# Optimization experiments

Measured on AMD Instinct MI355X. Metric: run time of the kernel, lower is better.

Reference implementation:

```python
import jax, jax.numpy as jnp
import numpy as np

N = 400_000   # active voxels
CIN = 64
COUT = 64
D = 192       # dense bounding volume side
K = 27        # 3x3x3 kernel taps


def _build_kmap():
    """Build per-tap neighbor index map [27, N], -1 where neighbor voxel is inactive.
    Mirrors fvdb's SparseConvPackInfo for stride=1, kernel=3, out_grid == in_grid."""
    rng = np.random.default_rng(0)
    coords = rng.integers(0, D, size=(int(N * 1.6), 3), dtype=np.int64)
    lin = coords[:, 0] * D * D + coords[:, 1] * D + coords[:, 2]
    lin = np.unique(lin)[:N]
    assert lin.shape[0] == N
    coords = np.stack([lin // (D * D), (lin // D) % D, lin % D], axis=1)
    lookup = np.full(D * D * D, -1, np.int32)
    lookup[lin] = np.arange(N, dtype=np.int32)
    nbr = np.full((K, N), -1, np.int32)
    k = 0
    for a in (-1, 0, 1):
        for b in (-1, 0, 1):
            for c in (-1, 0, 1):
                nc = coords + np.array([a, b, c])
                valid = np.all((nc >= 0) & (nc < D), axis=1)
                nlin = nc[:, 0] * D * D + nc[:, 1] * D + nc[:, 2]
                nbr[k, valid] = lookup[nlin[valid]]
                k += 1
    return jnp.asarray(nbr)


def setup_inputs() -> dict:
    key = jax.random.key(0)
    k1, k2, k3 = jax.random.split(key, 3)
    std = 1.0 / np.sqrt(CIN * K)  # reset_parameters: uniform(-std, std)
    feats = jax.random.normal(k1, (N, CIN), jnp.float32)
    weight = jax.random.uniform(k2, (K, CIN, COUT), jnp.float32, -std, std)
    bias = jax.random.uniform(k3, (COUT,), jnp.float32, -std, std)
    return {"feats": feats, "weight": weight, "bias": bias, "nbr_idx": _build_kmap()}


def reference(feats, weight, bias, nbr_idx):
    # Gather-scatter sparse conv: out[j] = bias + sum_k feats[nbr_k(j)] @ W[k]
    safe_idx = jnp.maximum(nbr_idx, 0)          # [K, N]
    valid = nbr_idx >= 0                        # [K, N]
    out0 = jnp.broadcast_to(bias, (N, COUT)).astype(feats.dtype)

    def tap(carry, xs):
        idx, msk, w = xs                        # [N], [N], [CIN, COUT]
        g = jnp.where(msk[:, None], feats[idx], 0.0)  # masked gather [N, CIN]
        return carry + g @ w, None

    out, _ = jax.lax.scan(tap, out0, (safe_idx, valid, weight))
    return out
```

## Files before the change

kernel.cpp:

```cpp
#include <hip/hip_runtime.h>
#include <stdint.h>

#define NVOX 400000
#define KTAPS 27

typedef __bf16 bf16x8 __attribute__((ext_vector_type(8)));
typedef float floatx16 __attribute__((ext_vector_type(16)));

__device__ __forceinline__ uint32_t f2bf(float f) {
  uint32_t u = __builtin_bit_cast(uint32_t, f);
  u += 0x7fffu + ((u >> 16) & 1u);
  return u >> 16;
}

__device__ __forceinline__ floatx16 zero16() {
  floatx16 z = {0.f,0.f,0.f,0.f,0.f,0.f,0.f,0.f,
                0.f,0.f,0.f,0.f,0.f,0.f,0.f,0.f};
  return z;
}

__global__ void k_wt(const float* __restrict__ W, unsigned short* __restrict__ Wt) {
  int i = blockIdx.x * 256 + threadIdx.x;
  int k = i >> 12;
  int rem = i & 4095;
  int ci = rem >> 6;
  int co = rem & 63;
  Wt[(k << 12) + (co << 6) + ci] = (unsigned short)f2bf(W[i]);
}

__global__ void k_feats(const float4* __restrict__ F, uint2* __restrict__ Fb) {
  int i0 = blockIdx.x * 1024 + threadIdx.x;
#pragma unroll
  for (int j = 0; j < 4; ++j) {
    int i = i0 + j * 256;
    float4 v = F[i];
    uint2 o;
    o.x = f2bf(v.x) | (f2bf(v.y) << 16);
    o.y = f2bf(v.z) | (f2bf(v.w) << 16);
    Fb[i] = o;
  }
}

template<bool FB>
__global__ __launch_bounds__(256, 3) void k_conv(
    const float* __restrict__ feats,
    const unsigned short* __restrict__ featsb,
    const unsigned short* __restrict__ Wt,
    const float* __restrict__ bias,
    const int* __restrict__ nbr,
    float* __restrict__ out) {

  __shared__ alignas(16) unsigned short lA[256 * 72];
  __shared__ alignas(16) unsigned short lB[64 * 72];

  const int t = threadIdx.x;
  const int w = t >> 6;
  const int l = t & 63;
  const int half = l >> 5;
  const int lm = l & 31;

  const int nwg = gridDim.x;
  const int q = nwg >> 3, r8 = nwg & 7;
  const int xcd = blockIdx.x & 7, hi = blockIdx.x >> 3;
  const int wg = (xcd < r8 ? xcd * (q + 1) : r8 * (q + 1) + (xcd - r8) * q) + hi;
  const int v0 = wg * 256;

  floatx16 acc00 = zero16(), acc01 = zero16(), acc10 = zero16(), acc11 = zero16();

  const unsigned short* pA0 = &lA[(w * 64 + lm) * 72 + half * 8];
  const unsigned short* pA1 = pA0 + 32 * 72;
  const unsigned short* pB0 = &lB[lm * 72 + half * 8];
  const unsigned short* pB1 = pB0 + 32 * 72;

  const int rr = t >> 3;
  const int cc = t & 7;

  int voff[8];
  bool vld[8];
#pragma unroll
  for (int p = 0; p < 8; ++p) {
    voff[p] = v0 + p * 32 + rr;
    vld[p] = voff[p] < NVOX;
  }
  const int brow = t >> 2;
  const int bcol = (t & 3) * 16;

  int idxA[8];
  int idxN[8];
  uint4 rA[8] = {{0,0,0,0},{0,0,0,0},{0,0,0,0},{0,0,0,0},
                 {0,0,0,0},{0,0,0,0},{0,0,0,0},{0,0,0,0}};
  uint4 rB0, rB1;

  auto gather = [&](int id) -> uint4 {
    int sid = id < 0 ? 0 : id;
    if (FB) {
      return *(const uint4*)(featsb + (size_t)sid * 64 + cc * 8);
    } else {
      const float* s = feats + (size_t)sid * 64 + cc * 8;
      float4 f0 = *(const float4*)s;
      float4 f1 = *(const float4*)(s + 4);
      uint4 d;
      d.x = f2bf(f0.x) | (f2bf(f0.y) << 16);
      d.y = f2bf(f0.z) | (f2bf(f0.w) << 16);
      d.z = f2bf(f1.x) | (f2bf(f1.y) << 16);
      d.w = f2bf(f1.z) | (f2bf(f1.w) << 16);
      return d;
    }
  };

#pragma unroll
  for (int p = 0; p < 8; ++p) idxN[p] = vld[p] ? nbr[voff[p]] : -1;
  {
    const unsigned short* src = Wt + brow * 64 + bcol;
    rB0 = *(const uint4*)src;
    rB1 = *(const uint4*)(src + 8);
  }
#pragma unroll
  for (int p = 0; p < 8; ++p) {
    int id = idxN[p];
    idxA[p] = id;
    if (id >= 0) rA[p] = gather(id);
  }
#pragma unroll
  for (int p = 0; p < 8; ++p) idxN[p] = vld[p] ? nbr[NVOX + voff[p]] : -1;

#pragma unroll 1
  for (int k = 0; k < KTAPS; ++k) {
    __syncthreads();

#pragma unroll
    for (int p = 0; p < 8; ++p) {
      uint4 v = rA[p];
      if (idxA[p] < 0) { v.x = 0u; v.y = 0u; v.z = 0u; v.w = 0u; }
      *(uint4*)&lA[(p * 32 + rr) * 72 + cc * 8] = v;
    }
    {
      unsigned short* dst = &lB[brow * 72 + bcol];
      *(uint4*)dst = rB0;
      *(uint4*)(dst + 8) = rB1;
    }
    __syncthreads();

    if (k + 1 < KTAPS) {
      const unsigned short* src = Wt + ((k + 1) << 12) + brow * 64 + bcol;
      rB0 = *(const uint4*)src;
      rB1 = *(const uint4*)(src + 8);
#pragma unroll
      for (int p = 0; p < 8; ++p) {
        int id = idxN[p];
        idxA[p] = id;
        if (id >= 0) rA[p] = gather(id);
      }
      if (k + 2 < KTAPS) {
        const int* nb = nbr + (size_t)(k + 2) * NVOX;
#pragma unroll
        for (int p = 0; p < 8; ++p) idxN[p] = vld[p] ? nb[voff[p]] : -1;
      }
    }

#pragma unroll
    for (int kc = 0; kc < 4; ++kc) {
      bf16x8 a0 = *(const bf16x8*)(pA0 + kc * 16);
      bf16x8 a1 = *(const bf16x8*)(pA1 + kc * 16);
      bf16x8 b0 = *(const bf16x8*)(pB0 + kc * 16);
      bf16x8 b1 = *(const bf16x8*)(pB1 + kc * 16);
      acc00 = __builtin_amdgcn_mfma_f32_32x32x16_bf16(a0, b0, acc00, 0, 0, 0);
      acc01 = __builtin_amdgcn_mfma_f32_32x32x16_bf16(a0, b1, acc01, 0, 0, 0);
      acc10 = __builtin_amdgcn_mfma_f32_32x32x16_bf16(a1, b0, acc10, 0, 0, 0);
      acc11 = __builtin_amdgcn_mfma_f32_32x32x16_bf16(a1, b1, acc11, 0, 0, 0);
    }
  }

  float bv0 = bias[lm];
  float bv1 = bias[32 + lm];
#pragma unroll
  for (int reg = 0; reg < 16; ++reg) {
    int m = (reg & 3) + 8 * (reg >> 2) + 4 * half;
    int vm0 = v0 + w * 64 + m;
    int vm1 = vm0 + 32;
    if (vm0 < NVOX) {
      out[vm0 * 64 + lm]      = acc00[reg] + bv0;
      out[vm0 * 64 + 32 + lm] = acc01[reg] + bv1;
    }
    if (vm1 < NVOX) {
      out[vm1 * 64 + lm]      = acc10[reg] + bv0;
      out[vm1 * 64 + 32 + lm] = acc11[reg] + bv1;
    }
  }
}

extern "C" void kernel_launch(void* const* d_in, const int* in_sizes, int n_in,
                              void* d_out, int out_size, void* d_ws, size_t ws_size,
                              hipStream_t stream) {
  const float* feats  = (const float*)d_in[0];
  const float* weight = (const float*)d_in[1];
  const float* bias   = (const float*)d_in[2];
  const int*   nbr    = (const int*)d_in[3];
  float* out = (float*)d_out;

  unsigned short* Wt = (unsigned short*)d_ws;
  const size_t featsOff = 256 * 1024;
  const size_t fbytes = (size_t)NVOX * 64 * 2;
  const bool bigws = ws_size >= featsOff + fbytes;

  k_wt<<<432, 256, 0, stream>>>(weight, Wt);

  const int grid = (NVOX + 255) / 256;
  if (bigws) {
    unsigned short* Fb = (unsigned short*)((char*)d_ws + featsOff);
    k_feats<<<6250, 256, 0, stream>>>((const float4*)feats, (uint2*)Fb);
    k_conv<true><<<grid, 256, 0, stream>>>(feats, Fb, Wt, bias, nbr, out);
  } else {
    k_conv<false><<<grid, 256, 0, stream>>>(feats, nullptr, Wt, bias, nbr, out);
  }
}
```

Before: 334.7 us.

## Load MFMA operands directly from global memory, dropping LDS staging and barriers

The conv kernel no longer stages gathered features and weights through shared memory. Each lane loads its MFMA A fragments straight from the bf16 feature rows, and its B fragments from a weight buffer pre-permuted into MFMA fragment order, which removes both __syncthreads per tap and the LDS round trips. The cost is that register-prefetch software pipelining is gone: gathers for tap k are issued in the same iteration that consumes them, leaving only the neighbor-index prefetch. Each wave now fetches the full weight tile itself, where before it was shared across the block.

```diff
diff --git a/kernel.cpp b/kernel.cpp
--- a/kernel.cpp
+++ b/kernel.cpp
@@ -19,13 +19,17 @@
   return z;
 }
 
-__global__ void k_wt(const float* __restrict__ W, unsigned short* __restrict__ Wt) {
-  int i = blockIdx.x * 256 + threadIdx.x;
-  int k = i >> 12;
-  int rem = i & 4095;
-  int ci = rem >> 6;
-  int co = rem & 63;
-  Wt[(k << 12) + (co << 6) + ci] = (unsigned short)f2bf(W[i]);
+__global__ void k_wt(const float* __restrict__ W, unsigned short* __restrict__ Wt2) {
+  int o = blockIdx.x * 256 + threadIdx.x;
+  int k = o >> 12;
+  int r = o & 4095;
+  int kc = r >> 10;
+  int q  = (r >> 9) & 1;
+  int l  = (r >> 3) & 63;
+  int e  = r & 7;
+  int ci = kc * 16 + ((l >> 5) << 3) + e;
+  int co = q * 32 + (l & 31);
+  Wt2[o] = (unsigned short)f2bf(W[(k << 12) + ci * 64 + co]);
 }
 
 __global__ void k_feats(const float4* __restrict__ F, uint2* __restrict__ Fb) {
@@ -45,13 +49,10 @@
 __global__ __launch_bounds__(256, 3) void k_conv(
     const float* __restrict__ feats,
     const unsigned short* __restrict__ featsb,
-    const unsigned short* __restrict__ Wt,
+    const unsigned short* __restrict__ Wt2,
     const float* __restrict__ bias,
     const int* __restrict__ nbr,
     float* __restrict__ out) {
-
-  __shared__ alignas(16) unsigned short lA[256 * 72];
-  __shared__ alignas(16) unsigned short lB[64 * 72];
 
   const int t = threadIdx.x;
   const int w = t >> 6;
@@ -65,110 +66,85 @@
   const int wg = (xcd < r8 ? xcd * (q + 1) : r8 * (q + 1) + (xcd - r8) * q) + hi;
   const int v0 = wg * 256;
 
+  const int g0 = v0 + w * 64 + lm;
+  const int g1 = g0 + 32;
+  const bool vld0 = g0 < NVOX;
+  const bool vld1 = g1 < NVOX;
+
   floatx16 acc00 = zero16(), acc01 = zero16(), acc10 = zero16(), acc11 = zero16();
 
-  const unsigned short* pA0 = &lA[(w * 64 + lm) * 72 + half * 8];
-  const unsigned short* pA1 = pA0 + 32 * 72;
-  const unsigned short* pB0 = &lB[lm * 72 + half * 8];
-  const unsigned short* pB1 = pB0 + 32 * 72;
+  const unsigned short* WB = Wt2 + l * 8;
+  const int hoff = half * 8;
 
-  const int rr = t >> 3;
-  const int cc = t & 7;
-
-  int voff[8];
-  bool vld[8];
-#pragma unroll
-  for (int p = 0; p < 8; ++p) {
-    voff[p] = v0 + p * 32 + rr;
-    vld[p] = voff[p] < NVOX;
-  }
-  const int brow = t >> 2;
-  const int bcol = (t & 3) * 16;
-
-  int idxA[8];
-  int idxN[8];
-  uint4 rA[8] = {{0,0,0,0},{0,0,0,0},{0,0,0,0},{0,0,0,0},
-                 {0,0,0,0},{0,0,0,0},{0,0,0,0},{0,0,0,0}};
-  uint4 rB0, rB1;
-
-  auto gather = [&](int id) -> uint4 {
-    int sid = id < 0 ? 0 : id;
-    if (FB) {
-      return *(const uint4*)(featsb + (size_t)sid * 64 + cc * 8);
-    } else {
-      const float* s = feats + (size_t)sid * 64 + cc * 8;
-      float4 f0 = *(const float4*)s;
-      float4 f1 = *(const float4*)(s + 4);
-      uint4 d;
-      d.x = f2bf(f0.x) | (f2bf(f0.y) << 16);
-      d.y = f2bf(f0.z) | (f2bf(f0.w) << 16);
-      d.z = f2bf(f1.x) | (f2bf(f1.y) << 16);
-      d.w = f2bf(f1.z) | (f2bf(f1.w) << 16);
-      return d;
-    }
-  };
-
-#pragma unroll
-  for (int p = 0; p < 8; ++p) idxN[p] = vld[p] ? nbr[voff[p]] : -1;
-  {
-    const unsigned short* src = Wt + brow * 64 + bcol;
-    rB0 = *(const uint4*)src;
-    rB1 = *(const uint4*)(src + 8);
-  }
-#pragma unroll
-  for (int p = 0; p < 8; ++p) {
-    int id = idxN[p];
-    idxA[p] = id;
-    if (id >= 0) rA[p] = gather(id);
-  }
-#pragma unroll
-  for (int p = 0; p < 8; ++p) idxN[p] = vld[p] ? nbr[NVOX + voff[p]] : -1;
+  int id0 = vld0 ? nbr[g0] : -1;
+  int id1 = vld1 ? nbr[g1] : -1;
 
 #pragma unroll 1
   for (int k = 0; k < KTAPS; ++k) {
-    __syncthreads();
+    const unsigned short* bp = WB + (k << 12);
+    uint4 b00 = *(const uint4*)(bp);
+    uint4 b01 = *(const uint4*)(bp + 512);
+    uint4 b10 = *(const uint4*)(bp + 1024);
+    uint4 b11 = *(const uint4*)(bp + 1536);
+    uint4 b20 = *(const uint4*)(bp + 2048);
+    uint4 b21 = *(const uint4*)(bp + 2560);
+    uint4 b30 = *(const uint4*)(bp + 3072);
+    uint4 b31 = *(const uint4*)(bp + 3584);
 
-#pragma unroll
-    for (int p = 0; p < 8; ++p) {
-      uint4 v = rA[p];
-      if (idxA[p] < 0) { v.x = 0u; v.y = 0u; v.z = 0u; v.w = 0u; }
-      *(uint4*)&lA[(p * 32 + rr) * 72 + cc * 8] = v;
-    }
-    {
-      unsigned short* dst = &lB[brow * 72 + bcol];
-      *(uint4*)dst = rB0;
-      *(uint4*)(dst + 8) = rB1;
-    }
-    __syncthreads();
-
-    if (k + 1 < KTAPS) {
-      const unsigned short* src = Wt + ((k + 1) << 12) + brow * 64 + bcol;
-      rB0 = *(const uint4*)src;
-      rB1 = *(const uint4*)(src + 8);
-#pragma unroll
-      for (int p = 0; p < 8; ++p) {
-        int id = idxN[p];
-        idxA[p] = id;
-        if (id >= 0) rA[p] = gather(id);
+    uint4 a00 = {0,0,0,0}, a01 = {0,0,0,0}, a02 = {0,0,0,0}, a03 = {0,0,0,0};
+    uint4 a10 = {0,0,0,0}, a11 = {0,0,0,0}, a12 = {0,0,0,0}, a13 = {0,0,0,0};
+    if (FB) {
+      if (id0 >= 0) {
+        const unsigned short* s = featsb + (size_t)id0 * 64 + hoff;
+        a00 = *(const uint4*)(s);
+        a01 = *(const uint4*)(s + 16);
+        a02 = *(const uint4*)(s + 32);
+        a03 = *(const uint4*)(s + 48);
       }
-      if (k + 2 < KTAPS) {
-        const int* nb = nbr + (size_t)(k + 2) * NVOX;
-#pragma unroll
-        for (int p = 0; p < 8; ++p) idxN[p] = vld[p] ? nb[voff[p]] : -1;
+      if (id1 >= 0) {
+        const unsigned short* s = featsb + (size_t)id1 * 64 + hoff;
+        a10 = *(const uint4*)(s);
+        a11 = *(const uint4*)(s + 16);
+        a12 = *(const uint4*)(s + 32);
+        a13 = *(const uint4*)(s + 48);
+      }
+    } else {
+      if (id0 >= 0) {
+        const float* s = feats + (size_t)id0 * 64 + hoff;
+#define CVT(dst, p) do { float4 f0_ = *(const float4*)(p); float4 f1_ = *(const float4*)((p) + 4); \
+        dst.x = f2bf(f0_.x) | (f2bf(f0_.y) << 16); dst.y = f2bf(f0_.z) | (f2bf(f0_.w) << 16);     \
+        dst.z = f2bf(f1_.x) | (f2bf(f1_.y) << 16); dst.w = f2bf(f1_.z) | (f2bf(f1_.w) << 16); } while (0)
+        CVT(a00, s); CVT(a01, s + 16); CVT(a02, s + 32); CVT(a03, s + 48);
+      }
+      if (id1 >= 0) {
+        const float* s = feats + (size_t)id1 * 64 + hoff;
+        CVT(a10, s); CVT(a11, s + 16); CVT(a12, s + 32); CVT(a13, s + 48);
+#undef CVT
       }
     }
 
-#pragma unroll
-    for (int kc = 0; kc < 4; ++kc) {
-      bf16x8 a0 = *(const bf16x8*)(pA0 + kc * 16);
-      bf16x8 a1 = *(const bf16x8*)(pA1 + kc * 16);
-      bf16x8 b0 = *(const bf16x8*)(pB0 + kc * 16);
-      bf16x8 b1 = *(const bf16x8*)(pB1 + kc * 16);
-      acc00 = __builtin_amdgcn_mfma_f32_32x32x16_bf16(a0, b0, acc00, 0, 0, 0);
-      acc01 = __builtin_amdgcn_mfma_f32_32x32x16_bf16(a0, b1, acc01, 0, 0, 0);
-      acc10 = __builtin_amdgcn_mfma_f32_32x32x16_bf16(a1, b0, acc10, 0, 0, 0);
-      acc11 = __builtin_amdgcn_mfma_f32_32x32x16_bf16(a1, b1, acc11, 0, 0, 0);
+    if (k + 1 < KTAPS) {
+      const int* nb = nbr + (size_t)(k + 1) * NVOX;
+      id0 = vld0 ? nb[g0] : -1;
+      id1 = vld1 ? nb[g1] : -1;
     }
+
+    acc00 = __builtin_amdgcn_mfma_f32_32x32x16_bf16(__builtin_bit_cast(bf16x8, a00), __builtin_bit_cast(bf16x8, b00), acc00, 0, 0, 0);
+    acc01 = __builtin_amdgcn_mfma_f32_32x32x16_bf16(__builtin_bit_cast(bf16x8, a00), __builtin_bit_cast(bf16x8, b01), acc01, 0, 0, 0);
+    acc10 = __builtin_amdgcn_mfma_f32_32x32x16_bf16(__builtin_bit_cast(bf16x8, a10), __builtin_bit_cast(bf16x8, b00), acc10, 0, 0, 0);
+    acc11 = __builtin_amdgcn_mfma_f32_32x32x16_bf16(__builtin_bit_cast(bf16x8, a10), __builtin_bit_cast(bf16x8, b01), acc11, 0, 0, 0);
+    acc00 = __builtin_amdgcn_mfma_f32_32x32x16_bf16(__builtin_bit_cast(bf16x8, a01), __builtin_bit_cast(bf16x8, b10), acc00, 0, 0, 0);
+    acc01 = __builtin_amdgcn_mfma_f32_32x32x16_bf16(__builtin_bit_cast(bf16x8, a01), __builtin_bit_cast(bf16x8, b11), acc01, 0, 0, 0);
+    acc10 = __builtin_amdgcn_mfma_f32_32x32x16_bf16(__builtin_bit_cast(bf16x8, a11), __builtin_bit_cast(bf16x8, b10), acc10, 0, 0, 0);
+    acc11 = __builtin_amdgcn_mfma_f32_32x32x16_bf16(__builtin_bit_cast(bf16x8, a11), __builtin_bit_cast(bf16x8, b11), acc11, 0, 0, 0);
+    acc00 = __builtin_amdgcn_mfma_f32_32x32x16_bf16(__builtin_bit_cast(bf16x8, a02), __builtin_bit_cast(bf16x8, b20), acc00, 0, 0, 0);
+    acc01 = __builtin_amdgcn_mfma_f32_32x32x16_bf16(__builtin_bit_cast(bf16x8, a02), __builtin_bit_cast(bf16x8, b21), acc01, 0, 0, 0);
+    acc10 = __builtin_amdgcn_mfma_f32_32x32x16_bf16(__builtin_bit_cast(bf16x8, a12), __builtin_bit_cast(bf16x8, b20), acc10, 0, 0, 0);
+    acc11 = __builtin_amdgcn_mfma_f32_32x32x16_bf16(__builtin_bit_cast(bf16x8, a12), __builtin_bit_cast(bf16x8, b21), acc11, 0, 0, 0);
+    acc00 = __builtin_amdgcn_mfma_f32_32x32x16_bf16(__builtin_bit_cast(bf16x8, a03), __builtin_bit_cast(bf16x8, b30), acc00, 0, 0, 0);
+    acc01 = __builtin_amdgcn_mfma_f32_32x32x16_bf16(__builtin_bit_cast(bf16x8, a03), __builtin_bit_cast(bf16x8, b31), acc01, 0, 0, 0);
+    acc10 = __builtin_amdgcn_mfma_f32_32x32x16_bf16(__builtin_bit_cast(bf16x8, a13), __builtin_bit_cast(bf16x8, b30), acc10, 0, 0, 0);
+    acc11 = __builtin_amdgcn_mfma_f32_32x32x16_bf16(__builtin_bit_cast(bf16x8, a13), __builtin_bit_cast(bf16x8, b31), acc11, 0, 0, 0);
   }
 
   float bv0 = bias[lm];
```

Result: slower. 348.0 us (+4.0%).
